# Performance work log

Hardware: AMD Instinct MI355X
Metric: run time of the kernel (lower is better)

The kernel has to match this reference:

```python
import jax, jax.numpy as jnp
import numpy as np

N_HEADS = 16
HEAD_SIZE = 64
N_EMBD = N_HEADS * HEAD_SIZE  # 1024
B, T = 4, 2048


def setup_inputs() -> dict:
    key = jax.random.key(0)
    kx, kq, kk, kv, kp = jax.random.split(key, 5)
    s = 1.0 / np.sqrt(N_EMBD)
    return {
        "x": jax.random.normal(kx, (B, T, N_EMBD), dtype=jnp.float32),
        "Wq": jax.random.normal(kq, (N_EMBD, N_HEADS * HEAD_SIZE), dtype=jnp.float32) * s,
        "Wk": jax.random.normal(kk, (N_EMBD, N_HEADS * HEAD_SIZE), dtype=jnp.float32) * s,
        "Wv": jax.random.normal(kv, (N_EMBD, N_HEADS * HEAD_SIZE), dtype=jnp.float32) * s,
        "Wp": jax.random.normal(kp, (N_HEADS * HEAD_SIZE, N_EMBD), dtype=jnp.float32) * s,
    }


def reference(x, Wq, Wk, Wv, Wp):
    Bb, Tt, C = x.shape
    H, hs = N_HEADS, HEAD_SIZE
    # QKV projections (no bias), split heads: (B, H, T, hs)
    q = (x @ Wq).reshape(Bb, Tt, H, hs).transpose(0, 2, 1, 3)
    k = (x @ Wk).reshape(Bb, Tt, H, hs).transpose(0, 2, 1, 3)
    v = (x @ Wv).reshape(Bb, Tt, H, hs).transpose(0, 2, 1, 3)
    scores = jnp.einsum("bhqd,bhkd->bhqk", q, k) / np.sqrt(hs).astype(np.float32)
    causal = jnp.tril(jnp.ones((Tt, Tt), dtype=bool))
    scores = jnp.where(causal, scores, -jnp.inf)
    attn = jax.nn.softmax(scores, axis=-1)  # dropout p=0 -> identity
    o = jnp.einsum("bhqk,bhkd->bhqd", attn, v)  # (B, H, T, hs)
    # Faithfully replicate torch's view/transpose/view sequence:
    o = o.reshape(Bb, Tt, H * hs)          # raw reshape of (B,H,T,hs) buffer
    o = jnp.swapaxes(o, 1, 2)               # (B, H*hs, T)
    o = o.reshape(Bb, Tt, H * hs)           # contiguous().view
    return o @ Wp
```

## Files before the change

kernel.cpp:

```cpp
#include <hip/hip_runtime.h>

typedef unsigned short ush;
typedef unsigned int u32;
typedef __attribute__((ext_vector_type(4))) float f32x4;
typedef __attribute__((ext_vector_type(8))) short short8;
typedef __attribute__((ext_vector_type(8))) ush ushx8;
typedef __attribute__((ext_vector_type(4))) ush ushx4;

#define GAS __attribute__((address_space(1)))
#define LAS __attribute__((address_space(3)))

__device__ __forceinline__ void gl_lds16(const void* g, void* l) {
  __builtin_amdgcn_global_load_lds((const GAS void*)g, (LAS void*)l, 16, 0, 0);
}

__device__ __forceinline__ ush f2bf(float f) {
  union { float f; unsigned int u; } x; x.f = f;
  unsigned int r = x.u + 0x7fffu + ((x.u >> 16) & 1u);
  return (ush)(r >> 16);
}
__device__ __forceinline__ u32 fbits(float f) {
  union { float f; u32 u; } x; x.f = f; return x.u;
}

#define NEG_BIG (-1.0e4f)
#define SCL 0.18033688f

__global__ __launch_bounds__(256) void k_convert_x(
    const float* __restrict__ X, ush* __restrict__ Xb) {
  int idx = blockIdx.x * 256 + threadIdx.x;
  int base = idx * 8;
  f32x4 a = *(const f32x4*)(X + base);
  f32x4 b = *(const f32x4*)(X + base + 4);
  ushx8 o;
#pragma unroll
  for (int q = 0; q < 4; ++q) { o[q] = f2bf(a[q]); o[4 + q] = f2bf(b[q]); }
  *(ushx8*)(Xb + base) = o;
}

__global__ __launch_bounds__(256) void k_transpose_w(
    const float* __restrict__ W0, const float* __restrict__ W1,
    const float* __restrict__ W2, const float* __restrict__ W3,
    ush* __restrict__ Wt) {
  __shared__ ush Ts[64][72];
  const int z = blockIdx.z;
  const float* W = (z == 0) ? W0 : (z == 1) ? W1 : (z == 2) ? W2 : W3;
  ush* Ot = Wt + (size_t)z * 1048576;
  const int k0 = blockIdx.x * 64, n0 = blockIdx.y * 64;
  const int rr = threadIdx.x >> 4, cc = threadIdx.x & 15;
#pragma unroll
  for (int i = 0; i < 4; ++i) {
    int row = i * 16 + rr;
    f32x4 v = *(const f32x4*)(W + (size_t)(k0 + row) * 1024 + n0 + cc * 4);
#pragma unroll
    for (int q = 0; q < 4; ++q) Ts[row][cc * 4 + q] = f2bf(v[q]);
  }
  __syncthreads();
#pragma unroll
  for (int i = 0; i < 4; ++i) {
    int n = i * 16 + rr;
    ushx4 o;
#pragma unroll
    for (int q = 0; q < 4; ++q) o[q] = Ts[cc * 4 + q][n];
    *(ushx4*)(Ot + (size_t)(n0 + n) * 1024 + k0 + cc * 4) = o;
  }
}

__global__ __launch_bounds__(256) void k_gemm_qkv(
    const ush* __restrict__ X, const ush* __restrict__ Wt, ush* __restrict__ QKV) {
  __shared__ __align__(16) ush sm[16384];
  ush* As = sm;
  ush* Bs = sm + 8192;
  const int tid = threadIdx.x;
  const int w = tid >> 6, l = tid & 63, lr = l & 15, lg = l >> 4;
  const int mt = blockIdx.x, nt = blockIdx.y;
  const int which = nt >> 3, n0 = (nt & 7) * 128;
  const ush* Ag = X + (size_t)mt * 128 * 1024;
  const ush* Bg = Wt + (size_t)which * 1048576 + (size_t)n0 * 1024;
  const int wr = (w >> 1) * 64, wc = (w & 1) * 64;
  f32x4 acc[4][4] = {};
  for (int k0 = 0; k0 < 1024; k0 += 64) {
#pragma unroll
    for (int it = 0; it < 4; ++it) {
      int c = it * 256 + tid;
      int row = c >> 3, c8 = (c & 7) * 8;
      gl_lds16(Ag + (size_t)row * 1024 + k0 + c8, As + c * 8);
      gl_lds16(Bg + (size_t)row * 1024 + k0 + c8, Bs + c * 8);
    }
    asm volatile("s_waitcnt vmcnt(0)" ::: "memory");
    __syncthreads();
    short8 fa[2][4], fb[2][4];
#pragma unroll
    for (int s = 0; s < 2; ++s)
#pragma unroll
      for (int i = 0; i < 4; ++i) {
        fa[s][i] = *(const short8*)(As + (wr + i * 16 + lr) * 64 + s * 32 + lg * 8);
        fb[s][i] = *(const short8*)(Bs + (wc + i * 16 + lr) * 64 + s * 32 + lg * 8);
      }
#pragma unroll
    for (int s = 0; s < 2; ++s)
#pragma unroll
      for (int mi = 0; mi < 4; ++mi)
#pragma unroll
        for (int ni = 0; ni < 4; ++ni)
          acc[mi][ni] = __builtin_amdgcn_mfma_f32_16x16x32_bf16(fa[s][mi], fb[s][ni], acc[mi][ni], 0, 0, 0);
    __syncthreads();
  }
  ush* Ct = sm;
#pragma unroll
  for (int mi = 0; mi < 4; ++mi)
#pragma unroll
    for (int ni = 0; ni < 4; ++ni)
#pragma unroll
      for (int j = 0; j < 4; ++j)
        Ct[(wr + mi * 16 + lg * 4 + j) * 128 + wc + ni * 16 + lr] = f2bf(acc[mi][ni][j]);
  __syncthreads();
  ush* Om = QKV + (size_t)which * 8388608;
  const int m0 = mt * 128, b = m0 >> 11, t0 = m0 & 2047, h0 = n0 >> 6;
#pragma unroll
  for (int it = 0; it < 8; ++it) {
    int c = it * 256 + tid;
    int half = c >> 10;
    int cc = c & 1023;
    int r = cc >> 3;
    int c8 = (cc & 7) * 8;
    ushx8 v = *(const ushx8*)(Ct + r * 128 + half * 64 + c8);
    *(ushx8*)(Om + ((size_t)(b * 16 + h0 + half) * 2048 + t0 + r) * 64 + c8) = v;
  }
}

__global__ __launch_bounds__(256) void k_transpose_v(
    const ush* __restrict__ V, ush* __restrict__ Vt) {
  __shared__ ush Ts[64][66];
  const int tt = blockIdx.x, bh = blockIdx.y;
  const ush* Vh = V + (size_t)bh * 131072 + tt * 4096;
  ush* Oh = Vt + (size_t)bh * 131072 + tt * 64;
  const int tid = threadIdx.x;
#pragma unroll
  for (int it = 0; it < 2; ++it) {
    int idx = it * 256 + tid;
    int row = idx >> 3, c8 = (idx & 7) * 8;
    ushx8 v = *(const ushx8*)(Vh + row * 64 + c8);
#pragma unroll
    for (int k2 = 0; k2 < 8; ++k2) Ts[row][c8 + k2] = v[k2];
  }
  __syncthreads();
#pragma unroll
  for (int it = 0; it < 2; ++it) {
    int idx = it * 256 + tid;
    int d = idx >> 3, c8 = (idx & 7) * 8;
    ushx8 o;
#pragma unroll
    for (int k2 = 0; k2 < 8; ++k2) o[k2] = Ts[c8 + k2][d];
    *(ushx8*)(Oh + (size_t)d * 2048 + c8) = o;
  }
}

__global__ __launch_bounds__(256) void k_attn(
    const ush* __restrict__ Q, const ush* __restrict__ K,
    const ush* __restrict__ Vg, ush* __restrict__ O) {
  __shared__ __align__(16) ush Ks[2][4096];
  __shared__ __align__(16) ush Vs[2][4096];
  __shared__ __align__(16) ush Pl[8][1024];
  const int lid = blockIdx.x + 16 * blockIdx.y;
  const int qta = (lid >> 3) & 15;
  const int bh  = ((lid >> 7) << 3) | (lid & 7);
  const int qtb = 31 - qta;
  const size_t hb = (size_t)bh * (2048 * 64);
  const ush* Qh = Q + hb;
  const ush* Kh = K + hb;
  const ush* Vh = Vg + hb;
  const int tid = threadIdx.x, w = tid >> 6, l = tid & 63, lr = l & 15, lg = l >> 4;
  const int q0a = qta * 64 + w * 16, q0b = qtb * 64 + w * 16;

  short8 qfa[2], qfb[2];
#pragma unroll
  for (int s = 0; s < 2; ++s) {
    qfa[s] = *(const short8*)(Qh + (size_t)(q0a + lr) * 64 + s * 32 + lg * 8);
    qfb[s] = *(const short8*)(Qh + (size_t)(q0b + lr) * 64 + s * 32 + lg * 8);
  }
  f32x4 acca[4] = {}, accb[4] = {};
  float la[4] = {0.f, 0.f, 0.f, 0.f}, lb[4] = {0.f, 0.f, 0.f, 0.f};

  int koff[2], voff[2];
#pragma unroll
  for (int it = 0; it < 2; ++it) {
    int ch = it * 256 + tid;
    int r = ch >> 3, g = ch & 7;
    koff[it] = r * 64 + ((g ^ (r & 7)) << 3);
    int keyv = ((r & 7) + (r >> 3)) & 7;
    voff[it] = r * 2048 + ((g ^ keyv) << 3);
  }
  auto issueStage = [&](int c, int buf) {
#pragma unroll
    for (int it = 0; it < 2; ++it) {
      int ch = it * 256 + tid;
      gl_lds16(Kh + (size_t)c * 4096 + koff[it], &Ks[buf][ch * 8]);
      gl_lds16(Vh + c * 64 + voff[it], &Vs[buf][ch * 8]);
    }
  };

  auto ctile = [&](const ush* Kc, const ush* Vc, const short8* qf,
                   f32x4* acc, float* lrow, bool diag, ush* PlW) {
    f32x4 sf[4] = {};
#pragma unroll
    for (int s = 0; s < 2; ++s)
#pragma unroll
      for (int f = 0; f < 4; ++f) {
        int kv = f * 16 + lr;
        short8 kf = *(const short8*)(Kc + kv * 64 + (((s * 4 + lg) ^ (kv & 7)) << 3));
        sf[f] = __builtin_amdgcn_mfma_f32_16x16x32_bf16(qf[s], kf, sf[f], 0, 0, 0);
      }
#pragma unroll
    for (int f = 0; f < 4; ++f)
#pragma unroll
      for (int j = 0; j < 4; ++j) {
        float vv = sf[f][j] * SCL;
        if (diag && (f * 16 + lr) > (w * 16 + lg * 4 + j)) vv = NEG_BIG;
        sf[f][j] = __builtin_amdgcn_exp2f(vv);
      }
#pragma unroll
    for (int j = 0; j < 4; ++j)
      lrow[j] += (sf[0][j] + sf[1][j]) + (sf[2][j] + sf[3][j]);
#pragma unroll
    for (int f = 0; f < 4; ++f)
#pragma unroll
      for (int j = 0; j < 4; ++j) {
        int q = lg * 4 + j;
        PlW[q * 64 + ((f * 16 + lr) ^ ((q & 7) << 3))] = (ush)(fbits(sf[f][j]) >> 16);
      }
#pragma unroll
    for (int s = 0; s < 2; ++s) {
      short8 pf = *(const short8*)(PlW + lr * 64 + (((s * 4 + lg) ^ (lr & 7)) << 3));
#pragma unroll
      for (int db = 0; db < 4; ++db) {
        int dv = db * 16 + lr;
        int keyv = ((dv & 7) + (dv >> 3)) & 7;
        short8 vf = *(const short8*)(Vc + dv * 64 + (((s * 4 + lg) ^ keyv) << 3));
        acc[db] = __builtin_amdgcn_mfma_f32_16x16x32_bf16(pf, vf, acc[db], 0, 0, 0);
      }
    }
  };

  issueStage(0, 0);
  int cur = 0;
  for (int c = 0; c <= qtb; ++c) {
    asm volatile("s_waitcnt vmcnt(0)" ::: "memory");
    __syncthreads();
    if (c < qtb) issueStage(c + 1, cur ^ 1);
    const ush* Kc = Ks[cur];
    const ush* Vc = Vs[cur];
    if (c <= qta) ctile(Kc, Vc, qfa, acca, la, c == qta, Pl[w]);
    ctile(Kc, Vc, qfb, accb, lb, c == qtb, Pl[4 + w]);
    __syncthreads();
    cur ^= 1;
  }

#pragma unroll
  for (int msk = 1; msk <= 8; msk <<= 1)
#pragma unroll
    for (int j = 0; j < 4; ++j) {
      la[j] += __shfl_xor(la[j], msk);
      lb[j] += __shfl_xor(lb[j], msk);
    }
  float ia[4], ib[4];
#pragma unroll
  for (int j = 0; j < 4; ++j) {
    ia[j] = __builtin_amdgcn_rcpf(la[j]);
    ib[j] = __builtin_amdgcn_rcpf(lb[j]);
  }
  ush* Oh = O + hb;
#pragma unroll
  for (int db = 0; db < 4; ++db)
#pragma unroll
    for (int j = 0; j < 4; ++j) {
      Oh[(size_t)(q0a + lg * 4 + j) * 64 + db * 16 + lr] = f2bf(acca[db][j] * ia[j]);
      Oh[(size_t)(q0b + lg * 4 + j) * 64 + db * 16 + lr] = f2bf(accb[db][j] * ib[j]);
    }
}

__global__ __launch_bounds__(256) void k_gather(const ush* __restrict__ Ob, ush* __restrict__ Mb) {
  __shared__ ush Ls[2][128][68];
  const int jh = blockIdx.x, tau = blockIdx.y, b = blockIdx.z;
  const int tid = threadIdx.x;
#pragma unroll
  for (int it = 0; it < 8; ++it) {
    int c = it * 256 + tid;
    int r = c >> 3, d8 = (c & 7) * 8;
    int esel = r >> 7, jlow = r & 127;
    ushx8 v = *(const ushx8*)(Ob +
        ((size_t)(b * 16 + jh + esel * 8) * 2048 + jlow * 16 + tau) * 64 + d8);
    *(ushx8*)(&Ls[esel][jlow][d8]) = v;
  }
  __syncthreads();
  const int wv = tid >> 6, l = tid & 63;
  const int e = wv >> 1, jhalf = wv & 1, d = l;
  ush* Mrow = Mb + (size_t)b * 2097152 +
              (size_t)(128 * tau + 2 * d + e) * 1024 + jh * 128 + jhalf * 64;
#pragma unroll
  for (int ch = 0; ch < 8; ++ch) {
    ushx8 v;
#pragma unroll
    for (int k = 0; k < 8; ++k) v[k] = Ls[e][jhalf * 64 + ch * 8 + k][d];
    *(ushx8*)(Mrow + ch * 8) = v;
  }
}

__global__ __launch_bounds__(256) void k_gemm_out(
    const ush* __restrict__ A, const ush* __restrict__ Bt, float* __restrict__ Out) {
  __shared__ __align__(16) ush sm[16384];
  ush* As = sm;
  ush* Bs = sm + 8192;
  const int tid = threadIdx.x;
  const int w = tid >> 6, l = tid & 63, lr = l & 15, lg = l >> 4;
  const int mt = blockIdx.x, nt = blockIdx.y;
  const int n0 = nt * 128;
  const ush* Ag = A + (size_t)mt * 128 * 1024;
  const ush* Bg = Bt + (size_t)n0 * 1024;
  const int wr = (w >> 1) * 64, wc = (w & 1) * 64;
  f32x4 acc[4][4] = {};
  for (int k0 = 0; k0 < 1024; k0 += 64) {
#pragma unroll
    for (int it = 0; it < 4; ++it) {
      int c = it * 256 + tid;
      int row = c >> 3, c8 = (c & 7) * 8;
      gl_lds16(Ag + (size_t)row * 1024 + k0 + c8, As + c * 8);
      gl_lds16(Bg + (size_t)row * 1024 + k0 + c8, Bs + c * 8);
    }
    asm volatile("s_waitcnt vmcnt(0)" ::: "memory");
    __syncthreads();
    short8 fa[2][4], fb[2][4];
#pragma unroll
    for (int s = 0; s < 2; ++s)
#pragma unroll
      for (int i = 0; i < 4; ++i) {
        fa[s][i] = *(const short8*)(As + (wr + i * 16 + lr) * 64 + s * 32 + lg * 8);
        fb[s][i] = *(const short8*)(Bs + (wc + i * 16 + lr) * 64 + s * 32 + lg * 8);
      }
#pragma unroll
    for (int s = 0; s < 2; ++s)
#pragma unroll
      for (int mi = 0; mi < 4; ++mi)
#pragma unroll
        for (int ni = 0; ni < 4; ++ni)
          acc[mi][ni] = __builtin_amdgcn_mfma_f32_16x16x32_bf16(fa[s][mi], fb[s][ni], acc[mi][ni], 0, 0, 0);
    __syncthreads();
  }
  const int m0 = mt * 128;
#pragma unroll
  for (int mi = 0; mi < 4; ++mi)
#pragma unroll
    for (int ni = 0; ni < 4; ++ni)
#pragma unroll
      for (int j = 0; j < 4; ++j)
        Out[(size_t)(m0 + wr + mi * 16 + lg * 4 + j) * 1024 + n0 + wc + ni * 16 + lr] =
            acc[mi][ni][j];
}

extern "C" void kernel_launch(void* const* d_in, const int* in_sizes, int n_in,
                              void* d_out, int out_size, void* d_ws, size_t ws_size,
                              hipStream_t stream) {
  const float* x  = (const float*)d_in[0];
  const float* wq = (const float*)d_in[1];
  const float* wk = (const float*)d_in[2];
  const float* wv = (const float*)d_in[3];
  const float* wp = (const float*)d_in[4];
  float* out = (float*)d_out;
  char* ws = (char*)d_ws;
  ush* xb  = (ush*)ws;
  ush* wt  = (ush*)(ws + 16777216);
  ush* qkv = (ush*)(ws + 25165824);
  ush* vtg = xb;
  ush* ob  = qkv;
  ush* mb  = xb;

  k_convert_x<<<dim3(4096), 256, 0, stream>>>(x, xb);
  k_transpose_w<<<dim3(16, 16, 4), 256, 0, stream>>>(wq, wk, wv, wp, wt);
  k_gemm_qkv<<<dim3(64, 24), 256, 0, stream>>>(xb, wt, qkv);
  k_transpose_v<<<dim3(32, 64), 256, 0, stream>>>(qkv + 16777216, vtg);
  k_attn<<<dim3(16, 64), 256, 0, stream>>>(qkv, qkv + 8388608, vtg, ob);
  k_gather<<<dim3(8, 16, 4), 256, 0, stream>>>(ob, mb);
  k_gemm_out<<<dim3(64, 8), 256, 0, stream>>>(mb, wt + 3145728, out);
}
```

Before: 218.4 us.

## Double-buffer and swizzle LDS in QKV and output GEMMs with 256x128 tiles

```diff
diff --git a/kernel.cpp b/kernel.cpp
--- a/kernel.cpp
+++ b/kernel.cpp
@@ -66,66 +66,104 @@
   }
 }
 
-__global__ __launch_bounds__(256) void k_gemm_qkv(
+__global__ __launch_bounds__(512, 2) void k_gemm_qkv(
     const ush* __restrict__ X, const ush* __restrict__ Wt, ush* __restrict__ QKV) {
-  __shared__ __align__(16) ush sm[16384];
-  ush* As = sm;
-  ush* Bs = sm + 8192;
+  __shared__ __align__(16) ush As_[2][16384];
+  __shared__ __align__(16) ush Bs_[2][8192];
   const int tid = threadIdx.x;
   const int w = tid >> 6, l = tid & 63, lr = l & 15, lg = l >> 4;
+  const int wm = w >> 2, wn = w & 3;
   const int mt = blockIdx.x, nt = blockIdx.y;
   const int which = nt >> 3, n0 = (nt & 7) * 128;
-  const ush* Ag = X + (size_t)mt * 128 * 1024;
+  const ush* Ag = X + (size_t)mt * 256 * 1024;
   const ush* Bg = Wt + (size_t)which * 1048576 + (size_t)n0 * 1024;
-  const int wr = (w >> 1) * 64, wc = (w & 1) * 64;
-  f32x4 acc[4][4] = {};
-  for (int k0 = 0; k0 < 1024; k0 += 64) {
-#pragma unroll
-    for (int it = 0; it < 4; ++it) {
-      int c = it * 256 + tid;
-      int row = c >> 3, c8 = (c & 7) * 8;
-      gl_lds16(Ag + (size_t)row * 1024 + k0 + c8, As + c * 8);
-      gl_lds16(Bg + (size_t)row * 1024 + k0 + c8, Bs + c * 8);
-    }
-    asm volatile("s_waitcnt vmcnt(0)" ::: "memory");
-    __syncthreads();
-    short8 fa[2][4], fb[2][4];
-#pragma unroll
-    for (int s = 0; s < 2; ++s)
-#pragma unroll
-      for (int i = 0; i < 4; ++i) {
-        fa[s][i] = *(const short8*)(As + (wr + i * 16 + lr) * 64 + s * 32 + lg * 8);
-        fb[s][i] = *(const short8*)(Bs + (wc + i * 16 + lr) * 64 + s * 32 + lg * 8);
-      }
-#pragma unroll
-    for (int s = 0; s < 2; ++s)
-#pragma unroll
-      for (int mi = 0; mi < 4; ++mi)
-#pragma unroll
-        for (int ni = 0; ni < 4; ++ni)
-          acc[mi][ni] = __builtin_amdgcn_mfma_f32_16x16x32_bf16(fa[s][mi], fb[s][ni], acc[mi][ni], 0, 0, 0);
-    __syncthreads();
-  }
-  ush* Ct = sm;
-#pragma unroll
-  for (int mi = 0; mi < 4; ++mi)
-#pragma unroll
-    for (int ni = 0; ni < 4; ++ni)
+  int aoff[4], boff[2];
+#pragma unroll
+  for (int it = 0; it < 4; ++it) {
+    int ch = it * 512 + tid, row = ch >> 3, g = ch & 7;
+    aoff[it] = row * 1024 + ((g ^ (row & 7)) << 3);
+  }
+#pragma unroll
+  for (int it = 0; it < 2; ++it) {
+    int ch = it * 512 + tid, row = ch >> 3, g = ch & 7;
+    boff[it] = row * 1024 + ((g ^ (row & 7)) << 3);
+  }
+  f32x4 acc[8][2] = {};
+
+  auto issueS = [&](int kt, int buf) {
+    const ush* Asrc = Ag + kt * 64;
+    const ush* Bsrc = Bg + kt * 64;
+#pragma unroll
+    for (int it = 0; it < 4; ++it)
+      gl_lds16(Asrc + aoff[it], &As_[buf][((size_t)it * 512 + tid) * 8]);
+#pragma unroll
+    for (int it = 0; it < 2; ++it)
+      gl_lds16(Bsrc + boff[it], &Bs_[buf][((size_t)it * 512 + tid) * 8]);
+  };
+
+  issueS(0, 0);
+  for (int t = 0; t < 16; ++t) {
+    if (t < 15) {
+      issueS(t + 1, (t + 1) & 1);
+      asm volatile("s_waitcnt vmcnt(6)" ::: "memory");
+    } else {
+      asm volatile("s_waitcnt vmcnt(0)" ::: "memory");
+    }
+    __syncthreads();
+    const ush* Ab = As_[t & 1];
+    const ush* Bb = Bs_[t & 1];
+    short8 fb[2][2];
+#pragma unroll
+    for (int ni = 0; ni < 2; ++ni)
+#pragma unroll
+      for (int kk = 0; kk < 2; ++kk) {
+        int row = wn * 32 + ni * 16 + lr;
+        fb[ni][kk] = *(const short8*)(Bb + row * 64 + (((kk * 4 + lg) ^ (row & 7)) << 3));
+      }
+#pragma unroll
+    for (int qm = 0; qm < 4; ++qm) {
+      short8 fa[2][2];
+#pragma unroll
+      for (int m2 = 0; m2 < 2; ++m2)
+#pragma unroll
+        for (int kk = 0; kk < 2; ++kk) {
+          int row = wm * 128 + (qm * 2 + m2) * 16 + lr;
+          fa[m2][kk] = *(const short8*)(Ab + row * 64 + (((kk * 4 + lg) ^ (row & 7)) << 3));
+        }
+      __builtin_amdgcn_s_setprio(1);
+#pragma unroll
+      for (int m2 = 0; m2 < 2; ++m2)
+#pragma unroll
+        for (int ni = 0; ni < 2; ++ni)
+#pragma unroll
+          for (int kk = 0; kk < 2; ++kk)
+            acc[qm * 2 + m2][ni] = __builtin_amdgcn_mfma_f32_16x16x32_bf16(
+                fa[m2][kk], fb[ni][kk], acc[qm * 2 + m2][ni], 0, 0, 0);
+      __builtin_amdgcn_s_setprio(0);
+    }
+    __syncthreads();
+  }
+  ush* Ct = &As_[0][0];
+#pragma unroll
+  for (int mi = 0; mi < 8; ++mi)
+#pragma unroll
+    for (int ni = 0; ni < 2; ++ni)
 #pragma unroll
       for (int j = 0; j < 4; ++j)
-        Ct[(wr + mi * 16 + lg * 4 + j) * 128 + wc + ni * 16 + lr] = f2bf(acc[mi][ni][j]);
+        Ct[(wm * 128 + mi * 16 + lg * 4 + j) * 128 + wn * 32 + ni * 16 + lr] =
+            f2bf(acc[mi][ni][j]);
   __syncthreads();
   ush* Om = QKV + (size_t)which * 8388608;
-  const int m0 = mt * 128, b = m0 >> 11, t0 = m0 & 2047, h0 = n0 >> 6;
+  const int m0 = mt * 256, b = m0 >> 11, t0 = m0 & 2047, h0 = n0 >> 6;
 #pragma unroll
   for (int it = 0; it < 8; ++it) {
-    int c = it * 256 + tid;
-    int half = c >> 10;
-    int cc = c & 1023;
+    int c = it * 512 + tid;
+    int hsel = c >> 11;
+    int cc = c & 2047;
     int r = cc >> 3;
     int c8 = (cc & 7) * 8;
-    ushx8 v = *(const ushx8*)(Ct + r * 128 + half * 64 + c8);
-    *(ushx8*)(Om + ((size_t)(b * 16 + h0 + half) * 2048 + t0 + r) * 64 + c8) = v;
+    ushx8 v = *(const ushx8*)(Ct + r * 128 + hsel * 64 + c8);
+    *(ushx8*)(Om + ((size_t)(b * 16 + h0 + hsel) * 2048 + t0 + r) * 64 + c8) = v;
   }
 }
 
@@ -306,55 +344,92 @@
   }
 }
 
-__global__ __launch_bounds__(256) void k_gemm_out(
+__global__ __launch_bounds__(512, 2) void k_gemm_out(
     const ush* __restrict__ A, const ush* __restrict__ Bt, float* __restrict__ Out) {
-  __shared__ __align__(16) ush sm[16384];
-  ush* As = sm;
-  ush* Bs = sm + 8192;
+  __shared__ __align__(16) ush As_[2][16384];
+  __shared__ __align__(16) ush Bs_[2][8192];
   const int tid = threadIdx.x;
   const int w = tid >> 6, l = tid & 63, lr = l & 15, lg = l >> 4;
+  const int wm = w >> 2, wn = w & 3;
   const int mt = blockIdx.x, nt = blockIdx.y;
   const int n0 = nt * 128;
-  const ush* Ag = A + (size_t)mt * 128 * 1024;
+  const ush* Ag = A + (size_t)mt * 256 * 1024;
   const ush* Bg = Bt + (size_t)n0 * 1024;
-  const int wr = (w >> 1) * 64, wc = (w & 1) * 64;
-  f32x4 acc[4][4] = {};
-  for (int k0 = 0; k0 < 1024; k0 += 64) {
-#pragma unroll
-    for (int it = 0; it < 4; ++it) {
-      int c = it * 256 + tid;
-      int row = c >> 3, c8 = (c & 7) * 8;
-      gl_lds16(Ag + (size_t)row * 1024 + k0 + c8, As + c * 8);
-      gl_lds16(Bg + (size_t)row * 1024 + k0 + c8, Bs + c * 8);
-    }
-    asm volatile("s_waitcnt vmcnt(0)" ::: "memory");
-    __syncthreads();
-    short8 fa[2][4], fb[2][4];
-#pragma unroll
-    for (int s = 0; s < 2; ++s)
-#pragma unroll
-      for (int i = 0; i < 4; ++i) {
-        fa[s][i] = *(const short8*)(As + (wr + i * 16 + lr) * 64 + s * 32 + lg * 8);
-        fb[s][i] = *(const short8*)(Bs + (wc + i * 16 + lr) * 64 + s * 32 + lg * 8);
-      }
-#pragma unroll
-    for (int s = 0; s < 2; ++s)
-#pragma unroll
-      for (int mi = 0; mi < 4; ++mi)
-#pragma unroll
-        for (int ni = 0; ni < 4; ++ni)
-          acc[mi][ni] = __builtin_amdgcn_mfma_f32_16x16x32_bf16(fa[s][mi], fb[s][ni], acc[mi][ni], 0, 0, 0);
-    __syncthreads();
-  }
-  const int m0 = mt * 128;
-#pragma unroll
-  for (int mi = 0; mi < 4; ++mi)
-#pragma unroll
-    for (int ni = 0; ni < 4; ++ni)
+  int aoff[4], boff[2];
+#pragma unroll
+  for (int it = 0; it < 4; ++it) {
+    int ch = it * 512 + tid, row = ch >> 3, g = ch & 7;
+    aoff[it] = row * 1024 + ((g ^ (row & 7)) << 3);
+  }
+#pragma unroll
+  for (int it = 0; it < 2; ++it) {
+    int ch = it * 512 + tid, row = ch >> 3, g = ch & 7;
+    boff[it] = row * 1024 + ((g ^ (row & 7)) << 3);
+  }
+  f32x4 acc[8][2] = {};
+
+  auto issueS = [&](int kt, int buf) {
+    const ush* Asrc = Ag + kt * 64;
+    const ush* Bsrc = Bg + kt * 64;
+#pragma unroll
+    for (int it = 0; it < 4; ++it)
+      gl_lds16(Asrc + aoff[it], &As_[buf][((size_t)it * 512 + tid) * 8]);
+#pragma unroll
+    for (int it = 0; it < 2; ++it)
+      gl_lds16(Bsrc + boff[it], &Bs_[buf][((size_t)it * 512 + tid) * 8]);
+  };
+
+  issueS(0, 0);
+  for (int t = 0; t < 16; ++t) {
+    if (t < 15) {
+      issueS(t + 1, (t + 1) & 1);
+      asm volatile("s_waitcnt vmcnt(6)" ::: "memory");
+    } else {
+      asm volatile("s_waitcnt vmcnt(0)" ::: "memory");
+    }
+    __syncthreads();
+    const ush* Ab = As_[t & 1];
+    const ush* Bb = Bs_[t & 1];
+    short8 fb[2][2];
+#pragma unroll
+    for (int ni = 0; ni < 2; ++ni)
+#pragma unroll
+      for (int kk = 0; kk < 2; ++kk) {
+        int row = wn * 32 + ni * 16 + lr;
+        fb[ni][kk] = *(const short8*)(Bb + row * 64 + (((kk * 4 + lg) ^ (row & 7)) << 3));
+      }
+#pragma unroll
+    for (int qm = 0; qm < 4; ++qm) {
+      short8 fa[2][2];
+#pragma unroll
+      for (int m2 = 0; m2 < 2; ++m2)
+#pragma unroll
+        for (int kk = 0; kk < 2; ++kk) {
+          int row = wm * 128 + (qm * 2 + m2) * 16 + lr;
+          fa[m2][kk] = *(const short8*)(Ab + row * 64 + (((kk * 4 + lg) ^ (row & 7)) << 3));
+        }
+      __builtin_amdgcn_s_setprio(1);
+#pragma unroll
+      for (int m2 = 0; m2 < 2; ++m2)
+#pragma unroll
+        for (int ni = 0; ni < 2; ++ni)
+#pragma unroll
+          for (int kk = 0; kk < 2; ++kk)
+            acc[qm * 2 + m2][ni] = __builtin_amdgcn_mfma_f32_16x16x32_bf16(
+                fa[m2][kk], fb[ni][kk], acc[qm * 2 + m2][ni], 0, 0, 0);
+      __builtin_amdgcn_s_setprio(0);
+    }
+    __syncthreads();
+  }
+  const int m0 = mt * 256;
+#pragma unroll
+  for (int mi = 0; mi < 8; ++mi)
+#pragma unroll
+    for (int ni = 0; ni < 2; ++ni)
 #pragma unroll
       for (int j = 0; j < 4; ++j)
-        Out[(size_t)(m0 + wr + mi * 16 + lg * 4 + j) * 1024 + n0 + wc + ni * 16 + lr] =
-            acc[mi][ni][j];
+        Out[(size_t)(m0 + wm * 128 + mi * 16 + lg * 4 + j) * 1024 +
+            n0 + wn * 32 + ni * 16 + lr] = acc[mi][ni][j];
 }
 
 extern "C" void kernel_launch(void* const* d_in, const int* in_sizes, int n_in,
@@ -376,9 +451,9 @@
 
   k_convert_x<<<dim3(4096), 256, 0, stream>>>(x, xb);
   k_transpose_w<<<dim3(16, 16, 4), 256, 0, stream>>>(wq, wk, wv, wp, wt);
-  k_gemm_qkv<<<dim3(64, 24), 256, 0, stream>>>(xb, wt, qkv);
+  k_gemm_qkv<<<dim3(32, 24), 512, 0, stream>>>(xb, wt, qkv);
   k_transpose_v<<<dim3(32, 64), 256, 0, stream>>>(qkv + 16777216, vtg);
   k_attn<<<dim3(16, 64), 256, 0, stream>>>(qkv, qkv + 8388608, vtg, ob);
   k_gather<<<dim3(8, 16, 4), 256, 0, stream>>>(ob, mb);
-  k_gemm_out<<<dim3(64, 8), 256, 0, stream>>>(mb, wt + 3145728, out);
-}
+  k_gemm_out<<<dim3(32, 8), 512, 0, stream>>>(mb, wt + 3145728, out);
+}
```

Result: no change. 215.2 us (-1.5%).
